# Kernel optimization log

Measured on AMD Instinct MI355X. Metric: run time of the kernel, lower is better.

Reference implementation:

```python
import jax, jax.numpy as jnp
import numpy as np

M, N, DIM = 32, 32, 128
BATCH = 2048
NITER = 100
ALPHA = 0.3
SIGMA = max(M, N) / 2.0


def setup_inputs() -> dict:
    key = jax.random.key(0)
    k1, k2 = jax.random.split(key)
    x = jax.random.normal(k1, (BATCH, DIM), dtype=jnp.float32)
    weights = jax.random.normal(k2, (M * N, DIM), dtype=jnp.float32)
    # Grid locations exactly as in the torch module (meshgrid, ravel, transpose)
    xx, yy = np.meshgrid(np.linspace(0, M - 1, M), np.linspace(0, N - 1, N))
    locations = jnp.asarray(
        np.array((xx.ravel(), yy.ravel())).T.astype(np.int32)
    )  # [mn, 2]
    return {"x": x, "weights": weights, "locations": locations, "it": 5}


def reference(x, weights, locations, it):
    # --- BMU search: pairwise Euclidean distances weights [mn,d] vs x [b,d] ---
    # argmin over squared distances == argmin over cdist (sqrt is monotone)
    w2 = jnp.sum(weights * weights, axis=1)  # [mn]
    x2 = jnp.sum(x * x, axis=1)              # [b]
    d2 = w2[:, None] + x2[None, :] - 2.0 * (weights @ x.T)  # [mn, b]
    bmu_idx = jnp.argmin(d2, axis=0)         # [b]
    bmu_locs = locations[bmu_idx]            # [b, 2]

    # --- linearly decayed learning rate / neighbourhood width ---
    lr_decay = 1.0 - it / NITER
    alpha_op = ALPHA * lr_decay
    sigma_op = SIGMA * lr_decay

    # --- gaussian neighbourhood over grid distances: [mn, b] ---
    locf = locations.astype(jnp.float32)
    bmuf = bmu_locs.astype(jnp.float32)
    bmu_d2 = jnp.sum((locf[:, None, :] - bmuf[None, :, :]) ** 2, axis=2)  # [mn, b]
    lr_op = alpha_op * jnp.exp(-bmu_d2 / (sigma_op * sigma_op))           # [mn, b]

    # --- delta = sum_b lr_op[:, b] * (x[b] - w)  (algebraically reduced) ---
    # == lr_op @ x - rowsum(lr_op) * weights; avoids the [mn, b, d] intermediate
    delta = lr_op @ x - jnp.sum(lr_op, axis=1, keepdims=True) * weights  # [mn, d]
    return weights + delta
```

## Files before the change

### kernel.cpp

```cpp
#include <hip/hip_runtime.h>
#include <stdint.h>

#define DIM   128
#define MN    1024
#define BATCH 2048
#define ALPHA 0.3f
#define SIGMA 16.0f
#define LOG2E 1.44269504088896f

typedef _Float16 half8 __attribute__((ext_vector_type(8)));
typedef float    floatx4 __attribute__((ext_vector_type(4)));


__global__ __launch_bounds__(1024) void bmu_kernel(
    const float* __restrict__ x, const float* __restrict__ w,
    unsigned long long* __restrict__ keys)
{
  __shared__ unsigned long long kb[16][16];

  const int t    = threadIdx.x;
  const int lane = t & 63;
  const int wv   = t >> 6;
  const int b0   = (blockIdx.x >> 1) * 16;
  const int h    = blockIdx.x & 1;
  const int r    = lane & 15;
  const int q    = lane >> 4;

  half8 Bh[4], Bl[4];
  {
    const float* xr = x + (b0 + r) * DIM + q * 8;
#pragma unroll
    for (int c = 0; c < 4; ++c) {
      float4 v0 = *reinterpret_cast<const float4*>(xr + c * 32);
      float4 v1 = *reinterpret_cast<const float4*>(xr + c * 32 + 4);
      float xs[8] = {v0.x, v0.y, v0.z, v0.w, v1.x, v1.y, v1.z, v1.w};
#pragma unroll
      for (int j = 0; j < 8; ++j) {
        _Float16 hh = (_Float16)xs[j];
        Bh[c][j] = hh;
        Bl[c][j] = (_Float16)(xs[j] - (float)hh);
      }
    }
  }

  unsigned long long kmin = ~0ull;
#pragma unroll
  for (int ut = 0; ut < 2; ++ut) {
    const int u0 = h * 512 + wv * 32 + ut * 16;
    half8 Ah[4], Al[4];
    float w2p = 0.f;
    {
      const float* wr = w + (u0 + r) * DIM + q * 8;
#pragma unroll
      for (int c = 0; c < 4; ++c) {
        float4 v0 = *reinterpret_cast<const float4*>(wr + c * 32);
        float4 v1 = *reinterpret_cast<const float4*>(wr + c * 32 + 4);
        float wsb[8] = {v0.x, v0.y, v0.z, v0.w, v1.x, v1.y, v1.z, v1.w};
#pragma unroll
        for (int j = 0; j < 8; ++j) {
          float vv = wsb[j];
          w2p = fmaf(vv, vv, w2p);
          _Float16 hh = (_Float16)vv;
          Ah[c][j] = hh;
          Al[c][j] = (_Float16)(vv - (float)hh);
        }
      }
    }
    w2p += __shfl_xor(w2p, 16);
    w2p += __shfl_xor(w2p, 32);

    floatx4 acc = {0.f, 0.f, 0.f, 0.f};
#pragma unroll
    for (int c = 0; c < 4; ++c) {
      acc = __builtin_amdgcn_mfma_f32_16x16x32_f16(Ah[c], Bh[c], acc, 0, 0, 0);
      acc = __builtin_amdgcn_mfma_f32_16x16x32_f16(Ah[c], Bl[c], acc, 0, 0, 0);
      acc = __builtin_amdgcn_mfma_f32_16x16x32_f16(Al[c], Bh[c], acc, 0, 0, 0);
    }
#pragma unroll
    for (int i = 0; i < 4; ++i) {
      float w2v = __shfl(w2p, q * 4 + i);
      float s = w2v - 2.0f * acc[i];
      unsigned int sb = __float_as_uint(s);
      sb ^= (sb >> 31) ? 0xFFFFFFFFu : 0x80000000u;
      unsigned long long key =
          ((unsigned long long)sb << 32) | (unsigned int)(u0 + q * 4 + i);
      if (key < kmin) kmin = key;
    }
  }
  unsigned long long o;
  o = __shfl_xor(kmin, 16); if (o < kmin) kmin = o;
  o = __shfl_xor(kmin, 32); if (o < kmin) kmin = o;
  if (lane < 16) kb[wv][r] = kmin;
  __syncthreads();
  if (t < 16) {
    unsigned long long m = kb[0][t];
#pragma unroll
    for (int k = 1; k < 16; ++k)
      if (kb[k][t] < m) m = kb[k][t];
    keys[h * BATCH + b0 + t] = m;
  }
}

#define PLANE 1064
__global__ __launch_bounds__(512) void convgather_kernel(
    const float* __restrict__ x, const unsigned long long* __restrict__ keys,
    const float* __restrict__ w, const int* __restrict__ itp,
    float* __restrict__ out)
{
  __shared__ float bin[4 * PLANE + 32 * 33];
  __shared__ float gxt[64], gyt[64];
  __shared__ float T1[4][32][4];
  __shared__ float Tcc[4][32];

  const int t   = threadIdx.x;
  const int q   = blockIdx.x >> 3;
  const int uxg = blockIdx.x & 7;

  for (int i = t; i < 4 * PLANE + 32 * 33; i += 512) bin[i] = 0.f;

  const float lr_decay = 1.0f - (float)itp[0] * 0.01f;
  const float alpha_op = ALPHA * lr_decay;
  const float sg       = SIGMA * lr_decay;
  const float c2       = -LOG2E / (sg * sg);
  if (t < 63) {
    float dd = (float)(t - 31);
    float g = __builtin_amdgcn_exp2f(c2 * dd * dd);
    gxt[t] = g;
    gyt[t] = alpha_op * g;
  }
  __syncthreads();

#pragma unroll
  for (int s = 0; s < 4; ++s) {
    int b = s * 512 + t;
    unsigned long long kA = keys[b];
    unsigned long long kB = keys[BATCH + b];
    unsigned int v = (unsigned int)(kA < kB ? kA : kB);
    int vy = v >> 5, vx = v & 31;
    float4 xv = *reinterpret_cast<const float4*>(&x[b * DIM + q * 4]);
    int base = vy * 33 + vx;
    atomicAdd(&bin[0 * PLANE + base], xv.x);
    atomicAdd(&bin[1 * PLANE + base], xv.y);
    atomicAdd(&bin[2 * PLANE + base], xv.z);
    atomicAdd(&bin[3 * PLANE + base], xv.w);
    atomicAdd(&bin[4 * PLANE + base], 1.0f);
  }
  __syncthreads();

  const int ui  = t >> 7;
  const int ux  = uxg * 4 + ui;
  const int rem = t & 127;
  const int vy  = rem >> 2;
  const int j   = rem & 3;

  {
    float a = 0.f, ac = 0.f;
    const float* Sp = bin + j * PLANE + vy * 33;
    const float* Cp = bin + 4 * PLANE + vy * 33;
#pragma unroll 8
    for (int vx = 0; vx < 32; ++vx) {
      float g = gxt[ux - vx + 31];
      a = fmaf(g, Sp[vx], a);
      if (j == 0) ac = fmaf(g, Cp[vx], ac);
    }
    T1[ui][vy][j] = a;
    if (j == 0) Tcc[ui][vy] = ac;
  }
  __syncthreads();

  {
    const int uy = vy;
    float d = 0.f, rs = 0.f;
#pragma unroll 8
    for (int v = 0; v < 32; ++v) {
      float g = gyt[uy - v + 31];
      d  = fmaf(g, T1[ui][v][j], d);
      rs = fmaf(g, Tcc[ui][v], rs);
    }
    int p = (uy * 32 + ux) * DIM + q * 4 + j;
    out[p] = w[p] * (1.0f - rs) + d;
  }
}

extern "C" void kernel_launch(void* const* d_in, const int* in_sizes, int n_in,
                              void* d_out, int out_size, void* d_ws, size_t ws_size,
                              hipStream_t stream) {
  const float* x   = (const float*)d_in[0];
  const float* w   = (const float*)d_in[1];
  const int*   itp = (const int*)d_in[3];
  float* out = (float*)d_out;

  unsigned long long* keys = (unsigned long long*)d_ws;

  bmu_kernel<<<256, 1024, 0, stream>>>(x, w, keys);
  convgather_kernel<<<256, 512, 0, stream>>>(x, keys, w, itp, out);
}
```

Baseline: 88.29 us.

## Fuse BMU binning into BMU kernel using global atomics and last-block merge

The BMU kernel now merges the two half-keys by letting whichever paired block arrives last, found through a global flag counter, finish the argmin. That block then scatters x rows into global per-cell sums and counts with atomics. The conv kernel just loads the precomputed sums instead of redoing the scatter in every one of its 256 blocks, removing redundant x reads and shared-memory atomics. In exchange it adds a memset launch, global float atomics that make the summation order nondeterministic, and a cross-block handoff that depends on acquire/release ordering.

```diff
diff --git a/kernel.cpp b/kernel.cpp
--- a/kernel.cpp
+++ b/kernel.cpp
@@ -11,17 +11,30 @@
 typedef _Float16 half8 __attribute__((ext_vector_type(8)));
 typedef float    floatx4 __attribute__((ext_vector_type(4)));
 
-
-__global__ __launch_bounds__(1024) void bmu_kernel(
+#define S_OFF    0
+#define CNT_OFF  (128 * 1024)
+#define FLAG_OFF (CNT_OFF + 1024)
+#define KEY_OFF  (FLAG_OFF + 128)
+#define MEMSET_BYTES (KEY_OFF * 4)
+
+__global__ __launch_bounds__(1024) void bmu_bin_kernel(
     const float* __restrict__ x, const float* __restrict__ w,
-    unsigned long long* __restrict__ keys)
+    float* __restrict__ ws)
 {
   __shared__ unsigned long long kb[16][16];
+  __shared__ unsigned int vcell[16];
+  __shared__ int oldflag;
+
+  float* S   = ws + S_OFF;
+  float* cnt = ws + CNT_OFF;
+  unsigned int* flags = (unsigned int*)(ws + FLAG_OFF);
+  unsigned long long* keys = (unsigned long long*)(ws + KEY_OFF);
 
   const int t    = threadIdx.x;
   const int lane = t & 63;
   const int wv   = t >> 6;
-  const int b0   = (blockIdx.x >> 1) * 16;
+  const int bg   = blockIdx.x >> 1;
+  const int b0   = bg * 16;
   const int h    = blockIdx.x & 1;
   const int r    = lane & 15;
   const int q    = lane >> 4;
@@ -92,20 +105,46 @@
   o = __shfl_xor(kmin, 32); if (o < kmin) kmin = o;
   if (lane < 16) kb[wv][r] = kmin;
   __syncthreads();
+
+  unsigned long long m = ~0ull;
   if (t < 16) {
-    unsigned long long m = kb[0][t];
+    m = kb[0][t];
 #pragma unroll
     for (int k = 1; k < 16; ++k)
       if (kb[k][t] < m) m = kb[k][t];
-    keys[h * BATCH + b0 + t] = m;
-  }
+    __hip_atomic_store(&keys[h * BATCH + b0 + t], m,
+                       __ATOMIC_RELAXED, __HIP_MEMORY_SCOPE_AGENT);
+  }
+  __syncthreads();
+
+  if (t == 0) {
+    oldflag = (int)__hip_atomic_fetch_add(&flags[bg], 1u,
+                  __ATOMIC_ACQ_REL, __HIP_MEMORY_SCOPE_AGENT);
+  }
+  __syncthreads();
+  if (oldflag == 0) return;
+
+  if (t < 16) {
+    unsigned long long pk = __hip_atomic_load(&keys[(h ^ 1) * BATCH + b0 + t],
+                               __ATOMIC_RELAXED, __HIP_MEMORY_SCOPE_AGENT);
+    if (pk < m) m = pk;
+    vcell[t] = (unsigned int)m;
+  }
+  __syncthreads();
+
+  const int bi = t >> 6;
+  const int d0 = (t & 63) * 2;
+  const unsigned int v = vcell[bi];
+  float2 xv = *reinterpret_cast<const float2*>(&x[(b0 + bi) * DIM + d0]);
+  atomicAdd(&S[d0 * MN + v], xv.x);
+  atomicAdd(&S[(d0 + 1) * MN + v], xv.y);
+  if ((t & 63) == 0) atomicAdd(&cnt[v], 1.0f);
 }
 
 #define PLANE 1064
-__global__ __launch_bounds__(512) void convgather_kernel(
-    const float* __restrict__ x, const unsigned long long* __restrict__ keys,
-    const float* __restrict__ w, const int* __restrict__ itp,
-    float* __restrict__ out)
+__global__ __launch_bounds__(512) void conv_kernel(
+    const float* __restrict__ ws, const float* __restrict__ w,
+    const int* __restrict__ itp, float* __restrict__ out)
 {
   __shared__ float bin[4 * PLANE + 32 * 33];
   __shared__ float gxt[64], gyt[64];
@@ -116,7 +155,18 @@
   const int q   = blockIdx.x >> 3;
   const int uxg = blockIdx.x & 7;
 
-  for (int i = t; i < 4 * PLANE + 32 * 33; i += 512) bin[i] = 0.f;
+  const float* Sq  = ws + S_OFF + (q * 4) * MN;
+  const float* cnt = ws + CNT_OFF;
+
+#pragma unroll
+  for (int i = t; i < 4096; i += 512) {
+    int j = i >> 10, v = i & 1023;
+    bin[j * PLANE + (v >> 5) * 33 + (v & 31)] = Sq[j * MN + v];
+  }
+#pragma unroll
+  for (int i = t; i < 1024; i += 512) {
+    bin[4 * PLANE + (i >> 5) * 33 + (i & 31)] = cnt[i];
+  }
 
   const float lr_decay = 1.0f - (float)itp[0] * 0.01f;
   const float alpha_op = ALPHA * lr_decay;
@@ -130,23 +180,6 @@
   }
   __syncthreads();
 
-#pragma unroll
-  for (int s = 0; s < 4; ++s) {
-    int b = s * 512 + t;
-    unsigned long long kA = keys[b];
-    unsigned long long kB = keys[BATCH + b];
-    unsigned int v = (unsigned int)(kA < kB ? kA : kB);
-    int vy = v >> 5, vx = v & 31;
-    float4 xv = *reinterpret_cast<const float4*>(&x[b * DIM + q * 4]);
-    int base = vy * 33 + vx;
-    atomicAdd(&bin[0 * PLANE + base], xv.x);
-    atomicAdd(&bin[1 * PLANE + base], xv.y);
-    atomicAdd(&bin[2 * PLANE + base], xv.z);
-    atomicAdd(&bin[3 * PLANE + base], xv.w);
-    atomicAdd(&bin[4 * PLANE + base], 1.0f);
-  }
-  __syncthreads();
-
   const int ui  = t >> 7;
   const int ux  = uxg * 4 + ui;
   const int rem = t & 127;
@@ -189,9 +222,9 @@
   const float* w   = (const float*)d_in[1];
   const int*   itp = (const int*)d_in[3];
   float* out = (float*)d_out;
-
-  unsigned long long* keys = (unsigned long long*)d_ws;
-
-  bmu_kernel<<<256, 1024, 0, stream>>>(x, w, keys);
-  convgather_kernel<<<256, 512, 0, stream>>>(x, keys, w, itp, out);
+  float* ws  = (float*)d_ws;
+
+  hipMemsetAsync(d_ws, 0, MEMSET_BYTES, stream);
+  bmu_bin_kernel<<<256, 1024, 0, stream>>>(x, w, ws);
+  conv_kernel<<<256, 512, 0, stream>>>(ws, w, itp, out);
 }
```

Result: slower. 96.00 us (+8.7%).

## Precompute fp16 hi/lo splits in a prep kernel and transpose x for binning

Applied to the files above, without the earlier changes.

Adds a prep kernel that converts weights and x into fp16 hi/lo fragments in MFMA-ready layout, computes weight norms once, and writes a column-blocked transposed copy of x. The BMU kernel then loads ready fragments and splits the codebook into four quarters across blocks, with two batch tiles per wave. The conv kernel reads coalesced transposed x and takes the minimum over four partial keys, using 1024 threads for binning. This removes the repeated per-block fp16 conversion and the strided x gathers, at the cost of an extra kernel launch and an extra round trip through the workspace.

```diff
diff --git a/kernel.cpp b/kernel.cpp
--- a/kernel.cpp
+++ b/kernel.cpp
@@ -11,101 +11,146 @@
 typedef _Float16 half8 __attribute__((ext_vector_type(8)));
 typedef float    floatx4 __attribute__((ext_vector_type(4)));
 
-
-__global__ __launch_bounds__(1024) void bmu_kernel(
+#define W_OFF   0
+#define X_OFF   (512 * 1024)
+#define XQ_OFF  (1536 * 1024)
+#define W2_OFF  (2560 * 1024)
+#define KEY_OFF (2564 * 1024)
+
+__global__ __launch_bounds__(1024) void prep_kernel(
     const float* __restrict__ x, const float* __restrict__ w,
-    unsigned long long* __restrict__ keys)
+    uint8_t* __restrict__ ws)
 {
-  __shared__ unsigned long long kb[16][16];
-
   const int t    = threadIdx.x;
   const int lane = t & 63;
   const int wv   = t >> 6;
-  const int b0   = (blockIdx.x >> 1) * 16;
-  const int h    = blockIdx.x & 1;
   const int r    = lane & 15;
   const int q    = lane >> 4;
-
-  half8 Bh[4], Bl[4];
-  {
-    const float* xr = x + (b0 + r) * DIM + q * 8;
+  const int bid  = blockIdx.x;
+
+  if (bid < 4) {
+    const int tu = bid * 16 + wv;
+    const float* wr = w + (tu * 16 + r) * DIM + q * 8;
+    uint8_t* Wc = ws + W_OFF + tu * 8192;
+    float w2p = 0.f;
 #pragma unroll
     for (int c = 0; c < 4; ++c) {
-      float4 v0 = *reinterpret_cast<const float4*>(xr + c * 32);
-      float4 v1 = *reinterpret_cast<const float4*>(xr + c * 32 + 4);
-      float xs[8] = {v0.x, v0.y, v0.z, v0.w, v1.x, v1.y, v1.z, v1.w};
+      float4 v0 = *reinterpret_cast<const float4*>(wr + c * 32);
+      float4 v1 = *reinterpret_cast<const float4*>(wr + c * 32 + 4);
+      float s[8] = {v0.x, v0.y, v0.z, v0.w, v1.x, v1.y, v1.z, v1.w};
+      half8 hh, ll;
 #pragma unroll
       for (int j = 0; j < 8; ++j) {
-        _Float16 hh = (_Float16)xs[j];
-        Bh[c][j] = hh;
-        Bl[c][j] = (_Float16)(xs[j] - (float)hh);
+        float vv = s[j];
+        w2p = fmaf(vv, vv, w2p);
+        _Float16 h = (_Float16)vv;
+        hh[j] = h;
+        ll[j] = (_Float16)(vv - (float)h);
       }
-    }
-  }
-
-  unsigned long long kmin = ~0ull;
-#pragma unroll
-  for (int ut = 0; ut < 2; ++ut) {
-    const int u0 = h * 512 + wv * 32 + ut * 16;
-    half8 Ah[4], Al[4];
-    float w2p = 0.f;
-    {
-      const float* wr = w + (u0 + r) * DIM + q * 8;
-#pragma unroll
-      for (int c = 0; c < 4; ++c) {
-        float4 v0 = *reinterpret_cast<const float4*>(wr + c * 32);
-        float4 v1 = *reinterpret_cast<const float4*>(wr + c * 32 + 4);
-        float wsb[8] = {v0.x, v0.y, v0.z, v0.w, v1.x, v1.y, v1.z, v1.w};
-#pragma unroll
-        for (int j = 0; j < 8; ++j) {
-          float vv = wsb[j];
-          w2p = fmaf(vv, vv, w2p);
-          _Float16 hh = (_Float16)vv;
-          Ah[c][j] = hh;
-          Al[c][j] = (_Float16)(vv - (float)hh);
-        }
-      }
+      *reinterpret_cast<half8*>(Wc + c * 2048 + lane * 16) = hh;
+      *reinterpret_cast<half8*>(Wc + c * 2048 + 1024 + lane * 16) = ll;
     }
     w2p += __shfl_xor(w2p, 16);
     w2p += __shfl_xor(w2p, 32);
-
+    if (q == 0)
+      reinterpret_cast<float*>(ws + W2_OFF)[tu * 16 + r] = w2p;
+  } else {
+    const int g  = (bid - 4) * 16 + wv;
+    const int tb = g >> 2, c = g & 3;
+    const int b  = tb * 16 + r;
+    const float* xr = x + b * DIM + q * 8 + c * 32;
+    float4 v0 = *reinterpret_cast<const float4*>(xr);
+    float4 v1 = *reinterpret_cast<const float4*>(xr + 4);
+    float s[8] = {v0.x, v0.y, v0.z, v0.w, v1.x, v1.y, v1.z, v1.w};
+    half8 hh, ll;
+#pragma unroll
+    for (int j = 0; j < 8; ++j) {
+      float vv = s[j];
+      _Float16 h = (_Float16)vv;
+      hh[j] = h;
+      ll[j] = (_Float16)(vv - (float)h);
+    }
+    uint8_t* Xc = ws + X_OFF + tb * 8192 + c * 2048;
+    *reinterpret_cast<half8*>(Xc + lane * 16) = hh;
+    *reinterpret_cast<half8*>(Xc + 1024 + lane * 16) = ll;
+    float4* XQ = reinterpret_cast<float4*>(ws + XQ_OFF);
+    XQ[(2 * q + 8 * c) * BATCH + b]     = v0;
+    XQ[(2 * q + 8 * c + 1) * BATCH + b] = v1;
+  }
+}
+
+__global__ __launch_bounds__(1024) void bmu_kernel(uint8_t* __restrict__ ws)
+{
+  __shared__ unsigned long long kb[16][2][16];
+
+  const int t    = threadIdx.x;
+  const int lane = t & 63;
+  const int wv   = t >> 6;
+  const int r    = lane & 15;
+  const int q    = lane >> 4;
+  const int bgrp = blockIdx.x >> 2;
+  const int qd   = blockIdx.x & 3;
+  const int tu   = qd * 16 + wv;
+  const int u0   = tu * 16;
+
+  const uint8_t* Wc = ws + W_OFF + tu * 8192;
+  half8 Ah[4], Al[4];
+#pragma unroll
+  for (int c = 0; c < 4; ++c) {
+    Ah[c] = *reinterpret_cast<const half8*>(Wc + c * 2048 + lane * 16);
+    Al[c] = *reinterpret_cast<const half8*>(Wc + c * 2048 + 1024 + lane * 16);
+  }
+  const float w2row = reinterpret_cast<const float*>(ws + W2_OFF)[u0 + r];
+
+  unsigned long long kmin[2] = {~0ull, ~0ull};
+#pragma unroll
+  for (int bt = 0; bt < 2; ++bt) {
+    const uint8_t* Xc = ws + X_OFF + (bgrp * 2 + bt) * 8192;
     floatx4 acc = {0.f, 0.f, 0.f, 0.f};
 #pragma unroll
     for (int c = 0; c < 4; ++c) {
-      acc = __builtin_amdgcn_mfma_f32_16x16x32_f16(Ah[c], Bh[c], acc, 0, 0, 0);
-      acc = __builtin_amdgcn_mfma_f32_16x16x32_f16(Ah[c], Bl[c], acc, 0, 0, 0);
-      acc = __builtin_amdgcn_mfma_f32_16x16x32_f16(Al[c], Bh[c], acc, 0, 0, 0);
+      half8 Bh = *reinterpret_cast<const half8*>(Xc + c * 2048 + lane * 16);
+      half8 Bl = *reinterpret_cast<const half8*>(Xc + c * 2048 + 1024 + lane * 16);
+      acc = __builtin_amdgcn_mfma_f32_16x16x32_f16(Ah[c], Bh, acc, 0, 0, 0);
+      acc = __builtin_amdgcn_mfma_f32_16x16x32_f16(Ah[c], Bl, acc, 0, 0, 0);
+      acc = __builtin_amdgcn_mfma_f32_16x16x32_f16(Al[c], Bh, acc, 0, 0, 0);
     }
 #pragma unroll
     for (int i = 0; i < 4; ++i) {
-      float w2v = __shfl(w2p, q * 4 + i);
+      float w2v = __shfl(w2row, q * 4 + i);
       float s = w2v - 2.0f * acc[i];
       unsigned int sb = __float_as_uint(s);
       sb ^= (sb >> 31) ? 0xFFFFFFFFu : 0x80000000u;
       unsigned long long key =
           ((unsigned long long)sb << 32) | (unsigned int)(u0 + q * 4 + i);
-      if (key < kmin) kmin = key;
-    }
-  }
-  unsigned long long o;
-  o = __shfl_xor(kmin, 16); if (o < kmin) kmin = o;
-  o = __shfl_xor(kmin, 32); if (o < kmin) kmin = o;
-  if (lane < 16) kb[wv][r] = kmin;
-  __syncthreads();
-  if (t < 16) {
-    unsigned long long m = kb[0][t];
-#pragma unroll
-    for (int k = 1; k < 16; ++k)
-      if (kb[k][t] < m) m = kb[k][t];
-    keys[h * BATCH + b0 + t] = m;
+      if (key < kmin[bt]) kmin[bt] = key;
+    }
+  }
+#pragma unroll
+  for (int bt = 0; bt < 2; ++bt) {
+    unsigned long long km = kmin[bt], o;
+    o = __shfl_xor(km, 16); if (o < km) km = o;
+    o = __shfl_xor(km, 32); if (o < km) km = o;
+    if (lane < 16) kb[wv][bt][r] = km;
+  }
+  __syncthreads();
+  if (t < 32) {
+    unsigned long long m = kb[0][t >> 4][t & 15];
+#pragma unroll
+    for (int k = 1; k < 16; ++k) {
+      unsigned long long v = kb[k][t >> 4][t & 15];
+      if (v < m) m = v;
+    }
+    unsigned long long* keys =
+        reinterpret_cast<unsigned long long*>(ws + KEY_OFF);
+    keys[qd * BATCH + bgrp * 32 + t] = m;
   }
 }
 
 #define PLANE 1064
-__global__ __launch_bounds__(512) void convgather_kernel(
-    const float* __restrict__ x, const unsigned long long* __restrict__ keys,
-    const float* __restrict__ w, const int* __restrict__ itp,
-    float* __restrict__ out)
+__global__ __launch_bounds__(1024) void conv_kernel(
+    const uint8_t* __restrict__ ws, const float* __restrict__ w,
+    const int* __restrict__ itp, float* __restrict__ out)
 {
   __shared__ float bin[4 * PLANE + 32 * 33];
   __shared__ float gxt[64], gyt[64];
@@ -116,7 +161,7 @@
   const int q   = blockIdx.x >> 3;
   const int uxg = blockIdx.x & 7;
 
-  for (int i = t; i < 4 * PLANE + 32 * 33; i += 512) bin[i] = 0.f;
+  for (int i = t; i < 4 * PLANE + 32 * 33; i += 1024) bin[i] = 0.f;
 
   const float lr_decay = 1.0f - (float)itp[0] * 0.01f;
   const float alpha_op = ALPHA * lr_decay;
@@ -130,14 +175,23 @@
   }
   __syncthreads();
 
-#pragma unroll
-  for (int s = 0; s < 4; ++s) {
-    int b = s * 512 + t;
-    unsigned long long kA = keys[b];
-    unsigned long long kB = keys[BATCH + b];
-    unsigned int v = (unsigned int)(kA < kB ? kA : kB);
+  const unsigned long long* keys =
+      reinterpret_cast<const unsigned long long*>(ws + KEY_OFF);
+  const float4* XQ =
+      reinterpret_cast<const float4*>(ws + XQ_OFF) + q * BATCH;
+#pragma unroll
+  for (int s = 0; s < 2; ++s) {
+    int b = s * 1024 + t;
+    unsigned long long k0 = keys[b];
+    unsigned long long k1 = keys[BATCH + b];
+    unsigned long long k2 = keys[2 * BATCH + b];
+    unsigned long long k3 = keys[3 * BATCH + b];
+    unsigned long long km = k0 < k1 ? k0 : k1;
+    if (k2 < km) km = k2;
+    if (k3 < km) km = k3;
+    unsigned int v = (unsigned int)km;
     int vy = v >> 5, vx = v & 31;
-    float4 xv = *reinterpret_cast<const float4*>(&x[b * DIM + q * 4]);
+    float4 xv = XQ[b];
     int base = vy * 33 + vx;
     atomicAdd(&bin[0 * PLANE + base], xv.x);
     atomicAdd(&bin[1 * PLANE + base], xv.y);
@@ -147,13 +201,12 @@
   }
   __syncthreads();
 
-  const int ui  = t >> 7;
-  const int ux  = uxg * 4 + ui;
-  const int rem = t & 127;
-  const int vy  = rem >> 2;
-  const int j   = rem & 3;
-
-  {
+  if (t < 512) {
+    const int ui  = t >> 7;
+    const int ux  = uxg * 4 + ui;
+    const int rem = t & 127;
+    const int vy  = rem >> 2;
+    const int j   = rem & 3;
     float a = 0.f, ac = 0.f;
     const float* Sp = bin + j * PLANE + vy * 33;
     const float* Cp = bin + 4 * PLANE + vy * 33;
@@ -168,8 +221,12 @@
   }
   __syncthreads();
 
-  {
-    const int uy = vy;
+  if (t < 512) {
+    const int ui  = t >> 7;
+    const int ux  = uxg * 4 + ui;
+    const int rem = t & 127;
+    const int uy  = rem >> 2;
+    const int j   = rem & 3;
     float d = 0.f, rs = 0.f;
 #pragma unroll 8
     for (int v = 0; v < 32; ++v) {
@@ -189,9 +246,9 @@
   const float* w   = (const float*)d_in[1];
   const int*   itp = (const int*)d_in[3];
   float* out = (float*)d_out;
-
-  unsigned long long* keys = (unsigned long long*)d_ws;
-
-  bmu_kernel<<<256, 1024, 0, stream>>>(x, w, keys);
-  convgather_kernel<<<256, 512, 0, stream>>>(x, keys, w, itp, out);
-}
+  uint8_t* ws = (uint8_t*)d_ws;
+
+  prep_kernel<<<36, 1024, 0, stream>>>(x, w, ws);
+  bmu_kernel<<<256, 1024, 0, stream>>>(ws);
+  conv_kernel<<<256, 1024, 0, stream>>>(ws, w, itp, out);
+}
```

Result: no change. 88.03 us (-0.3%).
